# Kernel optimization log

Hardware: AMD Instinct MI355X
Metric: run time of the kernel (lower is better)

The kernel has to match this reference:

```python
import jax, jax.numpy as jnp
import numpy as np

N, K, M, DIN, DOUT = 4096, 16, 65536, 256, 256


def setup_inputs() -> dict:
    key = jax.random.key(0)
    ks = jax.random.split(key, 16)
    s = 1.0 / np.sqrt(DOUT)
    x = jax.random.normal(ks[0], (N, DIN), jnp.float32)
    h_tensor = jax.random.normal(ks[1], (M, DOUT), jnp.float32)
    c_tensor = jax.random.normal(ks[2], (M, DOUT), jnp.float32)
    # variable-length child lists: lengths in [1, K], -1 padding like get_nums()
    lengths = jax.random.randint(ks[3], (N,), 1, K + 1)
    idx = jax.random.randint(ks[4], (N, K), 0, M)
    t = jnp.arange(K)[None, :]
    indice = jnp.where(t < lengths[:, None], idx, -1).astype(jnp.int32)
    W_w = jax.random.normal(ks[5], (4 * DOUT, DIN), jnp.float32) * s
    W_b = jax.random.normal(ks[6], (4 * DOUT,), jnp.float32) * s
    h0 = jax.random.normal(ks[7], (4, DOUT), jnp.float32)
    c0 = jax.random.normal(ks[8], (4, DOUT), jnp.float32)
    Wih = jax.random.normal(ks[9], (4, 2, 4 * DOUT, DOUT), jnp.float32) * s
    Whh = jax.random.normal(ks[10], (4, 2, 4 * DOUT, DOUT), jnp.float32) * s
    bih = jax.random.normal(ks[11], (4, 2, 4 * DOUT), jnp.float32) * s
    bhh = jax.random.normal(ks[12], (4, 2, 4 * DOUT), jnp.float32) * s
    fc = jax.random.normal(ks[13], (4, DOUT, 2 * DOUT), jnp.float32) * s
    return dict(x=x, h_tensor=h_tensor, c_tensor=c_tensor, indice=indice,
                W_w=W_w, W_b=W_b, h0=h0, c0=c0, Wih=Wih, Whh=Whh,
                bih=bih, bhh=bhh, fc=fc)


def _lstm_dir(xseq, mask, h_init, c_init, W_ih, W_hh, b, reverse):
    """Masked LSTM over child axis. xseq [N,K,d], mask [N,K] bool. Mimics
    pack_padded_sequence: state frozen and output 0 at padded steps."""
    d = h_init.shape[-1]
    xs = jnp.swapaxes(xseq, 0, 1)   # [K,N,d]
    ms = jnp.swapaxes(mask, 0, 1)   # [K,N]

    def step(carry, inp):
        h, c = carry
        xt, mt = inp
        g = xt @ W_ih.T + h @ W_hh.T + b        # [N,4d], gate order i,f,g,o
        i = jax.nn.sigmoid(g[:, :d])
        f = jax.nn.sigmoid(g[:, d:2 * d])
        u = jnp.tanh(g[:, 2 * d:3 * d])
        o = jax.nn.sigmoid(g[:, 3 * d:])
        c_new = f * c + i * u
        h_new = o * jnp.tanh(c_new)
        m = mt[:, None]
        return (jnp.where(m, h_new, h), jnp.where(m, c_new, c)), jnp.where(m, h_new, 0.0)

    _, ys = jax.lax.scan(step, (h_init, c_init), (xs, ms), reverse=reverse)
    return jnp.swapaxes(ys, 0, 1)   # [N,K,d]


def _bilstm_seq(xseq, mask, h0j, c0j, Wihj, Whhj, bihj, bhhj, fcj):
    n = xseq.shape[0]
    h_init = jnp.broadcast_to(h0j, (n, h0j.shape[-1]))
    c_init = jnp.broadcast_to(c0j, (n, c0j.shape[-1]))
    yf = _lstm_dir(xseq, mask, h_init, c_init, Wihj[0], Whhj[0], bihj[0] + bhhj[0], False)
    yb = _lstm_dir(xseq, mask, h_init, c_init, Wihj[1], Whhj[1], bihj[1] + bhhj[1], True)
    y = jnp.concatenate([yf, yb], axis=-1)      # [N,K,2d]
    return jnp.einsum('nkh,dh->nkd', y, fcj)    # fc (no bias); 0 stays 0 at pads


def reference(x, h_tensor, c_tensor, indice, W_w, W_b, h0, c0, Wih, Whh, bih, bhh, fc):
    mask = indice != -1                           # [N,K]
    length = mask.sum(axis=1)                     # [N], >= 1
    safe_idx = jnp.where(mask, indice, 0)
    h = h_tensor[safe_idx]                        # [N,K,d] gather of child states
    c = c_tensor[safe_idx]
    Wx = x @ W_w.T + W_b                          # [N,4d]
    d = DOUT
    Wf, Wi, Wu, Wo = Wx[:, :d], Wx[:, d:2 * d], Wx[:, 2 * d:3 * d], Wx[:, 3 * d:]
    ys = [_bilstm_seq(h, mask, h0[j], c0[j], Wih[j], Whh[j], bih[j], bhh[j], fc[j])
          for j in range(4)]                      # U_f, U_i, U_u, U_o
    # forget branch: per-child gate, masked sum over children
    branch_f_k = jax.nn.sigmoid(Wf[:, None, :] + ys[0])
    branch_f = jnp.sum(branch_f_k * c * mask[..., None], axis=1)
    # i/u/o use last valid timestep (packed LSTM y_last)
    ar = jnp.arange(x.shape[0])
    last = length - 1
    branch_i = jax.nn.sigmoid(ys[1][ar, last] + Wi)
    branch_u = jnp.tanh(ys[2][ar, last] + Wu)
    branch_o = jax.nn.sigmoid(ys[3][ar, last] + Wo)
    new_c = branch_i * branch_u + branch_f
    new_h = branch_o * jnp.tanh(new_c)
    return new_h, new_c
```

## Files before the change

### kernel.cpp

```cpp
#include <hip/hip_runtime.h>
#include <math.h>

#define N_SEQ 4096
#define KCH   16
#define DM    256
#define G4    1024
#define LP    40
#define EP    68

typedef __attribute__((ext_vector_type(8))) short bf8;
typedef __attribute__((ext_vector_type(4))) float f4;

__device__ __forceinline__ float fast_rcp(float x) { return __builtin_amdgcn_rcpf(x); }
__device__ __forceinline__ float sigf(float x)   { return fast_rcp(1.f + __expf(-x)); }
__device__ __forceinline__ float tanh_f(float x) { return 1.f - 2.f * fast_rcp(1.f + __expf(2.f * x)); }

__device__ __forceinline__ float bf2f(unsigned short u) {
    return __uint_as_float(((unsigned)u) << 16);
}
__device__ __forceinline__ unsigned short f2bf(float f) {
    unsigned u = __float_as_uint(f);
    unsigned r = (u + 0x7fffu + ((u >> 16) & 1u)) >> 16;
    return (unsigned short)r;
}
__device__ __forceinline__ unsigned pack2(float a, float b) {
    return (unsigned)f2bf(a) | ((unsigned)f2bf(b) << 16);
}

#define GLDS(gp, lp) __builtin_amdgcn_global_load_lds( \
    (const __attribute__((address_space(1))) void*)(gp), \
    (__attribute__((address_space(3))) void*)(lp), 16, 0, 0)

#define VW(n) asm volatile("s_waitcnt vmcnt(" #n ")" ::: "memory")

template<int NSEG, int LDB>
__device__ __forceinline__ void pass_pipe(
    const unsigned short* const (&segA)[NSEG],
    const unsigned short* const (&segB)[NSEG],
    unsigned short* SM,
    f4 (&acc)[4][4], int wave, int wm, int wn, int jq, int fr)
{
    constexpr int NS = NSEG * 8;
    constexpr int L  = 4;
    constexpr int NP = (NS < L) ? NS : L;

#pragma unroll
    for (int p = 0; p < NP; ++p) {
        const unsigned short* A_ = segA[p >> 3] + (p & 7) * 32;
        const unsigned short* B_ = segB[p >> 3] + (p & 7) * 32;
        unsigned short* a = SM + (p % 5) * 8192 + wave * 1024;
        unsigned short* b = a + 4096;
        GLDS(A_, a);        GLDS(A_ + 16 * DM, a + 512);
        GLDS(B_, b);        GLDS(B_ + 16 * LDB, b + 512);
    }
#pragma unroll
    for (int t = 0; t < NS; ++t) {
        const int rem = NS - 1 - t;
        if (rem >= 3)      VW(12);
        else if (rem == 2) VW(8);
        else if (rem == 1) VW(4);
        else               VW(0);
        __builtin_amdgcn_s_barrier();

        if (t + L < NS) {
            const int tn = t + L;
            const unsigned short* A_ = segA[tn >> 3] + (tn & 7) * 32;
            const unsigned short* B_ = segB[tn >> 3] + (tn & 7) * 32;
            unsigned short* a = SM + (tn % 5) * 8192 + wave * 1024;
            unsigned short* b = a + 4096;
            GLDS(A_, a);    GLDS(A_ + 16 * DM, a + 512);
            GLDS(B_, b);    GLDS(B_ + 16 * LDB, b + 512);
        }

        const unsigned short* Ab = SM + (t % 5) * 8192;
        const unsigned short* Bb = Ab + 4096;
        bf8 af[4], bb[4];
#pragma unroll
        for (int i = 0; i < 4; ++i)
            af[i] = *(const bf8*)(Ab + (wm + i * 16 + fr) * 32 + jq);
#pragma unroll
        for (int j = 0; j < 4; ++j)
            bb[j] = *(const bf8*)(Bb + (wn + j * 16 + fr) * 32 + jq);

        __builtin_amdgcn_s_setprio(1);
#pragma unroll
        for (int i = 0; i < 4; ++i)
#pragma unroll
            for (int j = 0; j < 4; ++j)
                acc[i][j] = __builtin_amdgcn_mfma_f32_16x16x32_bf16(
                    af[i], bb[j], acc[i][j], 0, 0, 0);
        __builtin_amdgcn_s_setprio(0);
    }
}

template<int KLEN>
__device__ __forceinline__ void pass_bf(
    const unsigned short* __restrict__ aRow,
    const unsigned short* __restrict__ bRow,
    unsigned short* Asm, unsigned short* Bsm, f4 (&acc)[4][4])
{
    const int tid  = threadIdx.x;
    const int kh   = (tid & 1) * 16;
    const int srow = tid >> 1;
    const int lane = tid & 63, wave = tid >> 6;
    const int wm = (wave >> 1) * 64, wn = (wave & 1) * 64;
    const int fr = lane & 15, fk = (lane >> 4) * 8;
    unsigned short* da = Asm + srow * LP + kh;
    unsigned short* db = Bsm + srow * LP + kh;

    for (int k0 = 0; k0 < KLEN; k0 += 32) {
        __syncthreads();
        *(int4*)(da)     = *(const int4*)(aRow + k0 + kh);
        *(int4*)(da + 8) = *(const int4*)(aRow + k0 + kh + 8);
        *(int4*)(db)     = *(const int4*)(bRow + k0 + kh);
        *(int4*)(db + 8) = *(const int4*)(bRow + k0 + kh + 8);
        __syncthreads();
        bf8 af[4], bb[4];
#pragma unroll
        for (int i = 0; i < 4; ++i)
            af[i] = *(const bf8*)(Asm + (wm + i * 16 + fr) * LP + fk);
#pragma unroll
        for (int j = 0; j < 4; ++j)
            bb[j] = *(const bf8*)(Bsm + (wn + j * 16 + fr) * LP + fk);
#pragma unroll
        for (int i = 0; i < 4; ++i)
#pragma unroll
            for (int j = 0; j < 4; ++j)
                acc[i][j] = __builtin_amdgcn_mfma_f32_16x16x32_bf16(
                    af[i], bb[j], acc[i][j], 0, 0, 0);
    }
}

template<int KLEN>
__device__ __forceinline__ void pass_f32(
    const float* __restrict__ aRow,
    const unsigned short* __restrict__ bRow,
    unsigned short* Asm, unsigned short* Bsm, f4 (&acc)[4][4])
{
    const int tid  = threadIdx.x;
    const int kh   = (tid & 1) * 16;
    const int srow = tid >> 1;
    const int lane = tid & 63, wave = tid >> 6;
    const int wm = (wave >> 1) * 64, wn = (wave & 1) * 64;
    const int fr = lane & 15, fk = (lane >> 4) * 8;
    unsigned short* da = Asm + srow * LP + kh;
    unsigned short* db = Bsm + srow * LP + kh;

    for (int k0 = 0; k0 < KLEN; k0 += 32) {
        __syncthreads();
        {
            const float* s = aRow + k0 + kh;
            float4 v0 = *(const float4*)(s);
            float4 v1 = *(const float4*)(s + 4);
            float4 v2 = *(const float4*)(s + 8);
            float4 v3 = *(const float4*)(s + 12);
            *(int4*)(da)     = make_int4(pack2(v0.x, v0.y), pack2(v0.z, v0.w),
                                         pack2(v1.x, v1.y), pack2(v1.z, v1.w));
            *(int4*)(da + 8) = make_int4(pack2(v2.x, v2.y), pack2(v2.z, v2.w),
                                         pack2(v3.x, v3.y), pack2(v3.z, v3.w));
        }
        *(int4*)(db)     = *(const int4*)(bRow + k0 + kh);
        *(int4*)(db + 8) = *(const int4*)(bRow + k0 + kh + 8);
        __syncthreads();
        bf8 af[4], bb[4];
#pragma unroll
        for (int i = 0; i < 4; ++i)
            af[i] = *(const bf8*)(Asm + (wm + i * 16 + fr) * LP + fk);
#pragma unroll
        for (int j = 0; j < 4; ++j)
            bb[j] = *(const bf8*)(Bsm + (wn + j * 16 + fr) * LP + fk);
#pragma unroll
        for (int i = 0; i < 4; ++i)
#pragma unroll
            for (int j = 0; j < 4; ++j)
                acc[i][j] = __builtin_amdgcn_mfma_f32_16x16x32_bf16(
                    af[i], bb[j], acc[i][j], 0, 0, 0);
    }
}


__global__ __launch_bounds__(256) void k_lastidx(
    const int* __restrict__ indice, int* __restrict__ last_idx)
{
    const int n = blockIdx.x * 256 + threadIdx.x;
    if (n >= N_SEQ) return;
    int len = 0;
#pragma unroll
    for (int k = 0; k < KCH; ++k) len += (indice[n * KCH + k] != -1);
    last_idx[n] = indice[n * KCH + (len - 1)];
}

__global__ __launch_bounds__(1024) void k_hh0_bsum2(
    const float* __restrict__ bih, const float* __restrict__ bhh,
    const float* __restrict__ h0, const float* __restrict__ Whh,
    float* __restrict__ bsum2)
{
    const int jz = blockIdx.x, j = jz + 1;
    const int g = threadIdx.x;
    const int jd = j * 2 + 1;
    const float* wrow = Whh + ((size_t)jd * G4 + g) * DM;
    float s = bih[jd * G4 + g] + bhh[jd * G4 + g];
    for (int h = 0; h < DM; ++h) s = fmaf(h0[j * DM + h], wrow[h], s);
    const int c = (g & 255) * 4 + (g >> 8);
    bsum2[jz * G4 + c] = s;
}

__global__ __launch_bounds__(256) void k_init_states(
    const float* __restrict__ h0, const float* __restrict__ c0,
    unsigned short* __restrict__ hA, float* __restrict__ c_state)
{
    const int row = blockIdx.x;
    const int s = row >> 12;
    const int tree = (s < 4) ? s : 0;
    const int d = threadIdx.x;
    hA[(size_t)row * DM + d]      = f2bf(h0[tree * DM + d]);
    c_state[(size_t)row * DM + d] = c0[tree * DM + d];
}

__global__ __launch_bounds__(256) void k_zero4(float4* __restrict__ p)
{
    p[(size_t)blockIdx.x * 256 + threadIdx.x] = make_float4(0.f, 0.f, 0.f, 0.f);
}

__global__ __launch_bounds__(256) void k_prep_wcat(
    const float* __restrict__ Wih, const float* __restrict__ Whh,
    const float* __restrict__ bih, const float* __restrict__ bhh,
    unsigned short* __restrict__ wcat, float* __restrict__ bsumr)
{
    const int c = blockIdx.x, s = blockIdx.y;
    const int wsel = (s < 4) ? s * 2 : 1;
    const int d = c >> 2, g = c & 3;
    const size_t srcrow = ((size_t)wsel * G4 + g * DM + d) * DM;
    unsigned short* dst = wcat + ((size_t)s * G4 + c) * 512;
    const int t = threadIdx.x;
    dst[t]       = f2bf(Wih[srcrow + t]);
    dst[256 + t] = f2bf(Whh[srcrow + t]);
    if (t == 0)
        bsumr[s * G4 + c] = bih[wsel * G4 + g * DM + d] + bhh[wsel * G4 + g * DM + d];
}

__global__ __launch_bounds__(256) void k_prep_wcat2(
    const float* __restrict__ Wih, unsigned short* __restrict__ wcat2)
{
    const int c = blockIdx.x, jz = blockIdx.y, j = jz + 1;
    const int d = c >> 2, g = c & 3;
    const size_t srcrow = ((size_t)(j * 2 + 1) * G4 + g * DM + d) * DM;
    wcat2[((size_t)jz * G4 + c) * 256 + threadIdx.x] = f2bf(Wih[srcrow + threadIdx.x]);
}

__global__ __launch_bounds__(256) void k_prep_fcb(
    const float* __restrict__ fc, unsigned short* __restrict__ fcb)
{
    const int dout = blockIdx.x, z = blockIdx.y, t = threadIdx.x;
    fcb[((size_t)z * DM + dout) * DM + t] = f2bf(fc[(size_t)dout * 512 + z * DM + t]);
}

__global__ __launch_bounds__(256) void k_prep_fcb2(
    const float* __restrict__ fc, unsigned short* __restrict__ fcb2)
{
    const int dout = blockIdx.x, jz = blockIdx.y, j = jz + 1, t = threadIdx.x;
    const float* src = fc + ((size_t)j * DM + dout) * 512;
    unsigned short* dst = fcb2 + ((size_t)jz * DM + dout) * 512;
    dst[t]       = f2bf(src[t]);
    dst[t + 256] = f2bf(src[t + 256]);
}

__global__ __launch_bounds__(256) void k_prep_wwb(
    const float* __restrict__ W_w, unsigned short* __restrict__ wwb)
{
    const size_t i = (size_t)blockIdx.x * 256 + threadIdx.x;
    wwb[i] = f2bf(W_w[i]);
}

__device__ __forceinline__ void gather_slice(
    const float* __restrict__ h_tensor, const int* __restrict__ indice,
    unsigned short* __restrict__ xbuf, int zz, int kk, int blk)
{
    const int row = blk * 64 + (threadIdx.x >> 2);
    const int cb  = (threadIdx.x & 3) * 64;
    int idx = indice[row * KCH + kk]; if (idx < 0) idx = 0;
    const float* src = h_tensor + (size_t)idx * DM + cb;
    unsigned short* dst = xbuf + ((size_t)zz * N_SEQ + row) * DM + cb;
#pragma unroll
    for (int c = 0; c < 64; c += 4) {
        float4 v = *(const float4*)(src + c);
        *(uint2*)(dst + c) = make_uint2(pack2(v.x, v.y), pack2(v.z, v.w));
    }
}

__global__ __launch_bounds__(256) void k_gather_x0(
    const float* __restrict__ h_tensor, const int* __restrict__ indice,
    unsigned short* __restrict__ xbuf)
{
    const int slice = blockIdx.x >> 6, blk = blockIdx.x & 63;
    gather_slice(h_tensor, indice, xbuf, slice, slice ? (KCH - 1) : 0, blk);
}

__global__ __launch_bounds__(256) void k_scan_merged(
    const unsigned short* __restrict__ xb_cur, unsigned short* __restrict__ xb_nxt,
    const unsigned short* __restrict__ yb_prev, unsigned short* __restrict__ yb_cur,
    const int* __restrict__ indice, const float* __restrict__ h_tensor,
    const unsigned short* __restrict__ h_in, unsigned short* __restrict__ h_out,
    float* __restrict__ c_state,
    const unsigned short* __restrict__ wcat, const float* __restrict__ bsumr,
    const unsigned short* __restrict__ fcb, unsigned short* __restrict__ ys0,
    int r)
{
    __shared__ __align__(16) unsigned short SMEM[40960];

    const int tid  = threadIdx.x;
    const int lane = tid & 63, wave = tid >> 6;
    const int wm = (wave >> 1) * 64, wn = (wave & 1) * 64;
    const int fr = lane & 15;
    const int jq = ((lane >> 4) ^ ((fr >> 1) & 3)) * 8;
    const int lr = wave * 32 + (lane >> 2);
    const int jl = ((lane & 3) ^ ((lane >> 3) & 3)) * 8;

    const int bz = blockIdx.z;

    if (bz == 5) {
        const int id5 = blockIdx.x + 8 * blockIdx.y;
        if (id5 >= 128) {
            const int rr = r + 1;
            if (rr >= KCH) return;
            const int g = id5 - 128;
            const int zz = g >> 6;
            gather_slice(h_tensor, indice, xb_nxt, zz,
                         zz ? (KCH - 1 - rr) : rr, g & 63);
            return;
        }
        if (r == 0) return;
        const int rp = r - 1;
        const int z = id5 >> 6;
        const int kslice = z ? (KCH - 1 - rp) : rp;
        const int row0 = (id5 & 31) * 128;
        const int c0 = ((id5 >> 5) & 1) * 128;

        const unsigned short* ay0 = yb_prev + ((size_t)z * N_SEQ + row0 + lr) * DM + jl;
        const unsigned short* bf0 = fcb + ((size_t)z * DM + c0 + lr) * DM + jl;

        f4 acc[4][4];
#pragma unroll
        for (int i = 0; i < 4; ++i)
#pragma unroll
            for (int j = 0; j < 4; ++j) acc[i][j] = (f4)(0.f);
        {
            const unsigned short* const segA[1] = { ay0 };
            const unsigned short* const segB[1] = { bf0 };
            pass_pipe<1, 256>(segA, segB, SMEM, acc, wave, wm, wn, jq, fr);
        }

#pragma unroll
        for (int i = 0; i < 4; ++i)
#pragma unroll
            for (int j = 0; j < 4; ++j) {
                const int col = c0 + wn + j * 16 + fr;
#pragma unroll
                for (int reg = 0; reg < 4; ++reg) {
                    const int rowg = row0 + wm + i * 16 + (lane >> 4) * 4 + reg;
                    const size_t ix = ((size_t)rowg * KCH + kslice) * DM + col;
                    ys0[ix] = f2bf(bf2f(ys0[ix]) + acc[i][j][reg]);
                }
            }
        return;
    }

    const int s = bz;
    const int k = (s < 4) ? r : (KCH - 1 - r);
    const int z = (s < 4) ? 0 : 1;
    const int bn = blockIdx.y & 7;
    const int bm = (blockIdx.y >> 3) * 8 + blockIdx.x;
    const int row0 = bm * 128, c0 = bn * 128;

    const unsigned short* xz = xb_cur + (size_t)z * N_SEQ * DM;
    const unsigned short* hs_in = h_in + (size_t)s * N_SEQ * DM;
    const unsigned short* ax0 = xz + (size_t)(row0 + lr) * DM + jl;
    const unsigned short* ah0 = hs_in + (size_t)(row0 + lr) * DM + jl;
    const unsigned short* bw0 = wcat + ((size_t)s * G4 + c0 + lr) * 512 + jl;

    f4 acc[4][4];
#pragma unroll
    for (int i = 0; i < 4; ++i)
#pragma unroll
        for (int j = 0; j < 4; ++j) acc[i][j] = (f4)(0.f);

    {
        const unsigned short* const segA[2] = { ax0, ah0 };
        const unsigned short* const segB[2] = { bw0, bw0 + 256 };
        pass_pipe<2, 512>(segA, segB, SMEM, acc, wave, wm, wn, jq, fr);
    }

    float* sc = (float*)SMEM + wave * (16 * EP);
    __syncthreads();
    const int kprev = (s < 4) ? (k - 1) : (k + 1);
    const int dq = lane & 15;
    const int rq = lane >> 4;
#pragma unroll
    for (int i = 0; i < 4; ++i) {
#pragma unroll
        for (int j = 0; j < 4; ++j) {
            const int colL = j * 16 + fr;
            const int rbase = (lane >> 4) * 4;
#pragma unroll
            for (int reg = 0; reg < 4; ++reg)
                sc[(rbase + reg) * EP + colL] = acc[i][j][reg];
        }
        asm volatile("s_waitcnt lgkmcnt(0)" ::: "memory");
        __builtin_amdgcn_sched_barrier(0);
#pragma unroll
        for (int q = 0; q < 4; ++q) {
            const int rloc = rq + q * 4;
            const int rowg = row0 + wm + i * 16 + rloc;
            const bool m = (indice[rowg * KCH + k] != -1);
            const bool mpv = (r == 0) ? true : (indice[rowg * KCH + kprev] != -1);
            const f4 gv = *(const f4*)(sc + rloc * EP + dq * 4);
            const f4 bb = *(const f4*)(bsumr + s * G4 + c0 + wn + dq * 4);
            const int d = ((c0 + wn) >> 2) + dq;
            const size_t cix = ((size_t)s * N_SEQ + rowg) * DM + d;
            unsigned short hv = 0;
            if (m) {
                const float ii = sigf(gv.x + bb.x);
                const float ff = sigf(gv.y + bb.y);
                const float uu = tanh_f(gv.z + bb.z);
                const float oo = sigf(gv.w + bb.w);
                const float c_old = c_state[cix];
                const float cn = ff * c_old + ii * uu;
                c_state[cix] = cn;
                hv = f2bf(oo * tanh_f(cn));
                h_out[cix] = hv;
            } else if (mpv) {
                h_out[cix] = hs_in[(size_t)rowg * DM + d];
            }
            if (s == 0)
                yb_cur[(size_t)rowg * DM + d] = m ? hv : (unsigned short)0;
            else if (s == 4)
                yb_cur[(size_t)(N_SEQ + rowg) * DM + d] = m ? hv : (unsigned short)0;
        }
        asm volatile("s_waitcnt lgkmcnt(0)" ::: "memory");
        __builtin_amdgcn_sched_barrier(0);
    }
}

__global__ __launch_bounds__(256) void k_acc_tail(
    const unsigned short* __restrict__ ybuf, const unsigned short* __restrict__ fcb,
    unsigned short* __restrict__ ys0)
{
    __shared__ __align__(16) unsigned short SMEM[40960];
    const int tid = threadIdx.x;
    const int lane = tid & 63, wave = tid >> 6;
    const int wm = (wave >> 1) * 64, wn = (wave & 1) * 64;
    const int fr = lane & 15;
    const int jq = ((lane >> 4) ^ ((fr >> 1) & 3)) * 8;
    const int lr = wave * 32 + (lane >> 2);
    const int jl = ((lane & 3) ^ ((lane >> 3) & 3)) * 8;

    const int z = blockIdx.z;
    const int kslice = z ? 0 : (KCH - 1);
    const int row0 = blockIdx.y * 128, c0 = blockIdx.x * 128;

    const unsigned short* ay0 = ybuf + ((size_t)z * N_SEQ + row0 + lr) * DM + jl;
    const unsigned short* bf0 = fcb + ((size_t)z * DM + c0 + lr) * DM + jl;

    f4 acc[4][4];
#pragma unroll
    for (int i = 0; i < 4; ++i)
#pragma unroll
        for (int j = 0; j < 4; ++j) acc[i][j] = (f4)(0.f);
    {
        const unsigned short* const segA[1] = { ay0 };
        const unsigned short* const segB[1] = { bf0 };
        pass_pipe<1, 256>(segA, segB, SMEM, acc, wave, wm, wn, jq, fr);
    }

#pragma unroll
    for (int i = 0; i < 4; ++i)
#pragma unroll
        for (int j = 0; j < 4; ++j) {
            const int col = c0 + wn + j * 16 + fr;
#pragma unroll
            for (int reg = 0; reg < 4; ++reg) {
                const int rowg = row0 + wm + i * 16 + (lane >> 4) * 4 + reg;
                const size_t ix = ((size_t)rowg * KCH + kslice) * DM + col;
                ys0[ix] = f2bf(bf2f(ys0[ix]) + acc[i][j][reg]);
            }
        }
}


__global__ __launch_bounds__(256) void k_bwd_mfma(
    const float* __restrict__ h_tensor, const int* __restrict__ last_idx,
    const unsigned short* __restrict__ wcat2, const float* __restrict__ bsum2,
    const float* __restrict__ c0, unsigned short* __restrict__ yb_last)
{
    __shared__ __align__(16) unsigned short SMEM[2 * 128 * LP];
    const int jz = blockIdx.z, j = jz + 1;
    const int row0 = blockIdx.y * 128, c0t = blockIdx.x * 128;
    const int tid = threadIdx.x;
    const int srow = tid >> 1;

    const float* aF = h_tensor + (size_t)last_idx[row0 + srow] * DM;
    const unsigned short* bR = wcat2 + ((size_t)jz * G4 + c0t + srow) * 256;

    f4 acc[4][4];
#pragma unroll
    for (int i = 0; i < 4; ++i)
#pragma unroll
        for (int jj = 0; jj < 4; ++jj) acc[i][jj] = (f4)(0.f);

    pass_f32<256>(aF, bR, SMEM, SMEM + 128 * LP, acc);

    const int lane = tid & 63, wave = tid >> 6;
    const int wm = (wave >> 1) * 64, wn = (wave & 1) * 64;
    float* sc = (float*)SMEM + wave * (16 * EP);

    __syncthreads();
#pragma unroll
    for (int i = 0; i < 4; ++i) {
#pragma unroll
        for (int jj = 0; jj < 4; ++jj) {
            const int colL = jj * 16 + (lane & 15);
            const int rbase = (lane >> 4) * 4;
#pragma unroll
            for (int reg = 0; reg < 4; ++reg)
                sc[(rbase + reg) * EP + colL] = acc[i][jj][reg];
        }
        __syncthreads();
        const int rowg = row0 + wm + i * 16 + (lane & 15);
#pragma unroll
        for (int q = 0; q < 4; ++q) {
            const int dL = (lane >> 4) + q * 4;
            const f4 gv = *(const f4*)(sc + (lane & 15) * EP + dL * 4);
            const f4 bb = *(const f4*)(bsum2 + jz * G4 + c0t + wn + dL * 4);
            const int d = ((c0t + wn) >> 2) + dL;
            const float ii = sigf(gv.x + bb.x);
            const float ff = sigf(gv.y + bb.y);
            const float uu = tanh_f(gv.z + bb.z);
            const float oo = sigf(gv.w + bb.w);
            const float cn = ff * c0[j * DM + d] + ii * uu;
            yb_last[((size_t)jz * N_SEQ + rowg) * DM + d] = f2bf(oo * tanh_f(cn));
        }
        __syncthreads();
    }
}

__global__ __launch_bounds__(256) void k_wx_mfma(
    const float* __restrict__ x, const unsigned short* __restrict__ wwb,
    const float* __restrict__ W_b, unsigned short* __restrict__ Wx)
{
    __shared__ __align__(16) unsigned short SMEM[2 * 128 * LP];
    const int row0 = blockIdx.y * 128, c0 = blockIdx.x * 128;
    const int tid = threadIdx.x;
    const int srow = tid >> 1;

    const float* aF = x + (size_t)(row0 + srow) * DM;
    const unsigned short* bR = wwb + (size_t)(c0 + srow) * DM;

    f4 acc[4][4];
#pragma unroll
    for (int i = 0; i < 4; ++i)
#pragma unroll
        for (int j = 0; j < 4; ++j) acc[i][j] = (f4)(0.f);

    pass_f32<256>(aF, bR, SMEM, SMEM + 128 * LP, acc);

    const int lane = tid & 63, wave = tid >> 6;
    const int wm = (wave >> 1) * 64, wn = (wave & 1) * 64;
#pragma unroll
    for (int i = 0; i < 4; ++i)
#pragma unroll
        for (int j = 0; j < 4; ++j) {
            const int col = c0 + wn + j * 16 + (lane & 15);
            const float bv = W_b[col];
#pragma unroll
            for (int reg = 0; reg < 4; ++reg) {
                const int rowg = row0 + wm + i * 16 + (lane >> 4) * 4 + reg;
                Wx[(size_t)rowg * G4 + col] = f2bf(acc[i][j][reg] + bv);
            }
        }
}

__global__ __launch_bounds__(256) void k_fc_last_mfma(
    const unsigned short* __restrict__ h_final, const unsigned short* __restrict__ yb_last,
    const unsigned short* __restrict__ fcb2, unsigned short* __restrict__ ys_last)
{
    __shared__ __align__(16) unsigned short SMEM[2 * 128 * LP];
    const int jz = blockIdx.z;
    const int row0 = blockIdx.y * 128, c0 = blockIdx.x * 128;
    const int tid = threadIdx.x;
    const int srow = tid >> 1;

    const unsigned short* aH1 = h_final + ((size_t)(1 + jz) * N_SEQ + row0 + srow) * DM;
    const unsigned short* aH2 = yb_last + ((size_t)jz * N_SEQ + row0 + srow) * DM;
    const unsigned short* bR  = fcb2 + ((size_t)jz * DM + c0 + srow) * 512;

    f4 acc[4][4];
#pragma unroll
    for (int i = 0; i < 4; ++i)
#pragma unroll
        for (int j = 0; j < 4; ++j) acc[i][j] = (f4)(0.f);

    pass_bf<256>(aH1, bR, SMEM, SMEM + 128 * LP, acc);
    pass_bf<256>(aH2, bR + 256, SMEM, SMEM + 128 * LP, acc);

    const int lane = tid & 63, wave = tid >> 6;
    const int wm = (wave >> 1) * 64, wn = (wave & 1) * 64;
#pragma unroll
    for (int i = 0; i < 4; ++i)
#pragma unroll
        for (int j = 0; j < 4; ++j) {
            const int col = c0 + wn + j * 16 + (lane & 15);
#pragma unroll
            for (int reg = 0; reg < 4; ++reg) {
                const int rowg = row0 + wm + i * 16 + (lane >> 4) * 4 + reg;
                ys_last[((size_t)jz * N_SEQ + rowg) * DM + col] = f2bf(acc[i][j][reg]);
            }
        }
}

__global__ __launch_bounds__(256) void k_final(
    const unsigned short* __restrict__ Wx, const unsigned short* __restrict__ ys0,
    const unsigned short* __restrict__ ys_last, const float* __restrict__ c_tensor,
    const int* __restrict__ indice, float* __restrict__ out)
{
    const int n = blockIdx.x, d = threadIdx.x;
    const float Wf = bf2f(Wx[(size_t)n * G4 + d]);
    const float Wi = bf2f(Wx[(size_t)n * G4 + DM + d]);
    const float Wu = bf2f(Wx[(size_t)n * G4 + 2 * DM + d]);
    const float Wo = bf2f(Wx[(size_t)n * G4 + 3 * DM + d]);
    float bf = 0.f;
#pragma unroll
    for (int k = 0; k < KCH; ++k) {
        const int id = indice[n * KCH + k];
        if (id >= 0)
            bf += sigf(Wf + bf2f(ys0[((size_t)n * KCH + k) * DM + d])) *
                  c_tensor[(size_t)id * DM + d];
    }
    const float bi = sigf(bf2f(ys_last[((size_t)0 * N_SEQ + n) * DM + d]) + Wi);
    const float bu = tanh_f(bf2f(ys_last[((size_t)1 * N_SEQ + n) * DM + d]) + Wu);
    const float bo = sigf(bf2f(ys_last[((size_t)2 * N_SEQ + n) * DM + d]) + Wo);
    const float nc = bi * bu + bf;
    const float nh = bo * tanh_f(nc);
    out[(size_t)n * DM + d] = nh;
    out[(size_t)N_SEQ * DM + (size_t)n * DM + d] = nc;
}

extern "C" void kernel_launch(void* const* d_in, const int* in_sizes, int n_in,
                              void* d_out, int out_size, void* d_ws, size_t ws_size,
                              hipStream_t stream)
{
    const float* x        = (const float*)d_in[0];
    const float* h_tensor = (const float*)d_in[1];
    const float* c_tensor = (const float*)d_in[2];
    const int*   indice   = (const int*)d_in[3];
    const float* W_w      = (const float*)d_in[4];
    const float* W_b      = (const float*)d_in[5];
    const float* h0       = (const float*)d_in[6];
    const float* c0       = (const float*)d_in[7];
    const float* Wih      = (const float*)d_in[8];
    const float* Whh      = (const float*)d_in[9];
    const float* bih      = (const float*)d_in[10];
    const float* bhh      = (const float*)d_in[11];
    const float* fc       = (const float*)d_in[12];
    float* out = (float*)d_out;

    char* base = (char*)d_ws;
    float*          c_state  = (float*)(base + 0);
    int*            last_idx = (int*)  (base + 20971520);
    float*          bsumr    = (float*)(base + 20987904);
    unsigned short* hA       = (unsigned short*)(base + 21008384);
    unsigned short* hB       = (unsigned short*)(base + 31494144);
    unsigned short* ys0      = (unsigned short*)(base + 41979904);
    unsigned short* ybufA    = (unsigned short*)(base + 75534336);
    unsigned short* ybufB    = (unsigned short*)(base + 79728640);
    unsigned short* xbufA    = (unsigned short*)(base + 83922944);
    unsigned short* fcb      = (unsigned short*)(base + 88117248);
    unsigned short* postbuf  = (unsigned short*)(base + 88379392);
    unsigned short* wcat     = (unsigned short*)(base + 92573696);
    const size_t need = 97816576;
    if (ws_size < need) return;

    unsigned short* xbufB   = postbuf;
    unsigned short* wcat2   = postbuf;
    unsigned short* fcb2    = postbuf + 786432;
    unsigned short* wwb     = postbuf + 1179648;
    float*          bsum2   = (float*)(postbuf + 1441792);
    unsigned short* yb_last = ybufA;
    unsigned short* ys_last = hB;
    unsigned short* WxBuf   = hA;

    k_lastidx<<<16, 256, 0, stream>>>(indice, last_idx);
    k_init_states<<<5 * N_SEQ, 256, 0, stream>>>(h0, c0, hA, c_state);
    k_zero4<<<8192, 256, 0, stream>>>((float4*)ys0);
    k_prep_wcat<<<dim3(G4, 5), 256, 0, stream>>>(Wih, Whh, bih, bhh, wcat, bsumr);
    k_prep_fcb<<<dim3(DM, 2), 256, 0, stream>>>(fc, fcb);
    k_gather_x0<<<128, 256, 0, stream>>>(h_tensor, indice, xbufA);

    for (int r = 0; r < KCH; ++r) {
        const unsigned short* xb_cur = (r & 1) ? xbufB : xbufA;
        unsigned short* xb_nxt       = (r & 1) ? xbufA : xbufB;
        const unsigned short* yb_prev = (r & 1) ? ybufA : ybufB;
        unsigned short* yb_cur        = (r & 1) ? ybufB : ybufA;
        const unsigned short* h_in = (r & 1) ? hB : hA;
        unsigned short* h_out      = (r & 1) ? hA : hB;
        k_scan_merged<<<dim3(8, 32, 6), 256, 0, stream>>>(
            xb_cur, xb_nxt, yb_prev, yb_cur, indice, h_tensor,
            h_in, h_out, c_state, wcat, bsumr, fcb, ys0, r);
    }

    k_acc_tail<<<dim3(2, 32, 2), 256, 0, stream>>>(ybufB, fcb, ys0);

    k_prep_wcat2<<<dim3(G4, 3), 256, 0, stream>>>(Wih, wcat2);
    k_hh0_bsum2<<<3, 1024, 0, stream>>>(bih, bhh, h0, Whh, bsum2);
    k_prep_fcb2<<<dim3(DM, 3), 256, 0, stream>>>(fc, fcb2);
    k_prep_wwb<<<1024, 256, 0, stream>>>(W_w, wwb);

    k_bwd_mfma<<<dim3(8, 32, 3), 256, 0, stream>>>(
        h_tensor, last_idx, wcat2, bsum2, c0, yb_last);
    k_fc_last_mfma<<<dim3(2, 32, 3), 256, 0, stream>>>(hA, yb_last, fcb2, ys_last);
    k_wx_mfma<<<dim3(8, 32), 256, 0, stream>>>(x, wwb, W_b, WxBuf);

    k_final<<<N_SEQ, 256, 0, stream>>>(WxBuf, ys0, ys_last, c_tensor, indice, out);
}
```

Before: 1.213 ms.

## Switch recurrent LSTM scan GEMMs to FP8 MFMA with scaled operands

Stores the gathered child inputs, hidden states and concatenated LSTM weights as scaled FP8 (e4m3) instead of bf16, and runs the main recurrent gate GEMM with the fp8 16x16x32 MFMA. Gate results are rescaled by a constant. Final hidden states are also written as bf16 into a separate buffer for the later fc kernel. The fc-accumulate pass moves to a simpler double-buffered pipeline. This halves operand bandwidth and LDS traffic in the 16-step scan, at the cost of lower numerical precision in the recurrence, which may exceed tolerance.

After: 1.298 ms. 7.0% more time.

```diff
diff --git a/kernel.cpp b/kernel.cpp
--- a/kernel.cpp
+++ b/kernel.cpp
@@ -7,6 +7,7 @@
 #define G4    1024
 #define LP    40
 #define EP    68
+#define GSC   0.0078125f
 
 typedef __attribute__((ext_vector_type(8))) short bf8;
 typedef __attribute__((ext_vector_type(4))) float f4;
@@ -26,12 +27,131 @@
 __device__ __forceinline__ unsigned pack2(float a, float b) {
     return (unsigned)f2bf(a) | ((unsigned)f2bf(b) << 16);
 }
+__device__ __forceinline__ unsigned char f2fp8(float x) {
+    return (unsigned char)(__builtin_amdgcn_cvt_pk_fp8_f32(x, 0.f, 0, false) & 0xff);
+}
+__device__ __forceinline__ unsigned pack4fp8(float a, float b, float c, float d) {
+    unsigned p = __builtin_amdgcn_cvt_pk_fp8_f32(a, b, 0, false);
+    return __builtin_amdgcn_cvt_pk_fp8_f32(c, d, p, true);
+}
+__device__ __forceinline__ float fp8dec(unsigned char u) {
+    const int e = (u >> 3) & 15, m = u & 7;
+    float v = (e == 0) ? (float)m * 0.001953125f
+                       : (float)(8 + m) * __uint_as_float((unsigned)(e + 117) << 23);
+    return (u & 0x80) ? -v : v;
+}
 
 #define GLDS(gp, lp) __builtin_amdgcn_global_load_lds( \
     (const __attribute__((address_space(1))) void*)(gp), \
     (__attribute__((address_space(3))) void*)(lp), 16, 0, 0)
 
 #define VW(n) asm volatile("s_waitcnt vmcnt(" #n ")" ::: "memory")
+
+template<int NSEG>
+__device__ __forceinline__ void pass_pipe8(
+    const unsigned char* const (&segA)[NSEG],
+    const unsigned char* const (&segB)[NSEG],
+    unsigned char* SM8,
+    f4 (&acc)[4][4], int wave, int wm, int wn, int lane)
+{
+    constexpr int NS = NSEG * 8;
+    constexpr int L  = 4;
+    constexpr int NP = (NS < L) ? NS : L;
+    const int fr = lane & 15, kh = (lane >> 4) * 8;
+
+#pragma unroll
+    for (int p = 0; p < NP; ++p) {
+        const unsigned char* A_ = segA[p >> 3] + (p & 7) * 32;
+        const unsigned char* B_ = segB[p >> 3] + (p & 7) * 32;
+        unsigned char* a = SM8 + (p % 5) * 8192 + wave * 1024;
+        unsigned char* b = a + 4096;
+        GLDS(A_, a);  GLDS(B_, b);
+    }
+#pragma unroll
+    for (int t = 0; t < NS; ++t) {
+        const int rem = NS - 1 - t;
+        if (rem >= 3)      VW(6);
+        else if (rem == 2) VW(4);
+        else if (rem == 1) VW(2);
+        else               VW(0);
+        __builtin_amdgcn_s_barrier();
+
+        if (t + L < NS) {
+            const int tn = t + L;
+            const unsigned char* A_ = segA[tn >> 3] + (tn & 7) * 32;
+            const unsigned char* B_ = segB[tn >> 3] + (tn & 7) * 32;
+            unsigned char* a = SM8 + (tn % 5) * 8192 + wave * 1024;
+            unsigned char* b = a + 4096;
+            GLDS(A_, a);  GLDS(B_, b);
+        }
+
+        const unsigned char* Ab = SM8 + (t % 5) * 8192;
+        const unsigned char* Bb = Ab + 4096;
+        long af[4], bb[4];
+#pragma unroll
+        for (int i = 0; i < 4; ++i)
+            af[i] = *(const long*)(Ab + (wm + i * 16 + fr) * 32 + kh);
+#pragma unroll
+        for (int j = 0; j < 4; ++j)
+            bb[j] = *(const long*)(Bb + (wn + j * 16 + fr) * 32 + kh);
+
+        __builtin_amdgcn_s_setprio(1);
+#pragma unroll
+        for (int i = 0; i < 4; ++i)
+#pragma unroll
+            for (int j = 0; j < 4; ++j)
+                acc[i][j] = __builtin_amdgcn_mfma_f32_16x16x32_fp8_fp8(
+                    af[i], bb[j], acc[i][j], 0, 0, 0);
+        __builtin_amdgcn_s_setprio(0);
+    }
+}
+
+template<int NSEG, int LDB>
+__device__ __forceinline__ void pass_pipe2(
+    const unsigned short* const (&segA)[NSEG],
+    const unsigned short* const (&segB)[NSEG],
+    unsigned short* SM,
+    f4 (&acc)[4][4], int wave, int wm, int wn, int jq, int fr)
+{
+    constexpr int NS = NSEG * 8;
+    {
+        const unsigned short* A_ = segA[0];
+        const unsigned short* B_ = segB[0];
+        unsigned short* a = SM + wave * 1024;
+        unsigned short* b = a + 4096;
+        GLDS(A_, a);        GLDS(A_ + 16 * DM, a + 512);
+        GLDS(B_, b);        GLDS(B_ + 16 * LDB, b + 512);
+    }
+#pragma unroll
+    for (int t = 0; t < NS; ++t) {
+        VW(0);
+        __builtin_amdgcn_s_barrier();
+        if (t + 1 < NS) {
+            const int tn = t + 1;
+            const unsigned short* A_ = segA[tn >> 3] + (tn & 7) * 32;
+            const unsigned short* B_ = segB[tn >> 3] + (tn & 7) * 32;
+            unsigned short* a = SM + (tn & 1) * 8192 + wave * 1024;
+            unsigned short* b = a + 4096;
+            GLDS(A_, a);    GLDS(A_ + 16 * DM, a + 512);
+            GLDS(B_, b);    GLDS(B_ + 16 * LDB, b + 512);
+        }
+        const unsigned short* Ab = SM + (t & 1) * 8192;
+        const unsigned short* Bb = Ab + 4096;
+        bf8 af[4], bb[4];
+#pragma unroll
+        for (int i = 0; i < 4; ++i)
+            af[i] = *(const bf8*)(Ab + (wm + i * 16 + fr) * 32 + jq);
+#pragma unroll
+        for (int j = 0; j < 4; ++j)
+            bb[j] = *(const bf8*)(Bb + (wn + j * 16 + fr) * 32 + jq);
+#pragma unroll
+        for (int i = 0; i < 4; ++i)
+#pragma unroll
+            for (int j = 0; j < 4; ++j)
+                acc[i][j] = __builtin_amdgcn_mfma_f32_16x16x32_bf16(
+                    af[i], bb[j], acc[i][j], 0, 0, 0);
+    }
+}
 
 template<int NSEG, int LDB>
 __device__ __forceinline__ void pass_pipe(
@@ -43,7 +163,6 @@
     constexpr int NS = NSEG * 8;
     constexpr int L  = 4;
     constexpr int NP = (NS < L) ? NS : L;
-
 #pragma unroll
     for (int p = 0; p < NP; ++p) {
         const unsigned short* A_ = segA[p >> 3] + (p & 7) * 32;
@@ -61,7 +180,6 @@
         else if (rem == 1) VW(4);
         else               VW(0);
         __builtin_amdgcn_s_barrier();
-
         if (t + L < NS) {
             const int tn = t + L;
             const unsigned short* A_ = segA[tn >> 3] + (tn & 7) * 32;
@@ -71,7 +189,6 @@
             GLDS(A_, a);    GLDS(A_ + 16 * DM, a + 512);
             GLDS(B_, b);    GLDS(B_ + 16 * LDB, b + 512);
         }
-
         const unsigned short* Ab = SM + (t % 5) * 8192;
         const unsigned short* Bb = Ab + 4096;
         bf8 af[4], bb[4];
@@ -81,7 +198,6 @@
 #pragma unroll
         for (int j = 0; j < 4; ++j)
             bb[j] = *(const bf8*)(Bb + (wn + j * 16 + fr) * 32 + jq);
-
         __builtin_amdgcn_s_setprio(1);
 #pragma unroll
         for (int i = 0; i < 4; ++i)
@@ -207,13 +323,13 @@
 
 __global__ __launch_bounds__(256) void k_init_states(
     const float* __restrict__ h0, const float* __restrict__ c0,
-    unsigned short* __restrict__ hA, float* __restrict__ c_state)
+    unsigned char* __restrict__ hA8, float* __restrict__ c_state)
 {
     const int row = blockIdx.x;
     const int s = row >> 12;
     const int tree = (s < 4) ? s : 0;
     const int d = threadIdx.x;
-    hA[(size_t)row * DM + d]      = f2bf(h0[tree * DM + d]);
+    hA8[(size_t)row * DM + d]     = f2fp8(h0[tree * DM + d] * 8.f);
     c_state[(size_t)row * DM + d] = c0[tree * DM + d];
 }
 
@@ -225,16 +341,16 @@
 __global__ __launch_bounds__(256) void k_prep_wcat(
     const float* __restrict__ Wih, const float* __restrict__ Whh,
     const float* __restrict__ bih, const float* __restrict__ bhh,
-    unsigned short* __restrict__ wcat, float* __restrict__ bsumr)
+    unsigned char* __restrict__ wcat8, float* __restrict__ bsumr)
 {
     const int c = blockIdx.x, s = blockIdx.y;
     const int wsel = (s < 4) ? s * 2 : 1;
     const int d = c >> 2, g = c & 3;
     const size_t srcrow = ((size_t)wsel * G4 + g * DM + d) * DM;
-    unsigned short* dst = wcat + ((size_t)s * G4 + c) * 512;
+    unsigned char* dst = wcat8 + ((size_t)s * G4 + c) * 512;
     const int t = threadIdx.x;
-    dst[t]       = f2bf(Wih[srcrow + t]);
-    dst[256 + t] = f2bf(Whh[srcrow + t]);
+    dst[t]       = f2fp8(Wih[srcrow + t] * 16.f);
+    dst[256 + t] = f2fp8(Whh[srcrow + t] * 16.f);
     if (t == 0)
         bsumr[s * G4 + c] = bih[wsel * G4 + g * DM + d] + bhh[wsel * G4 + g * DM + d];
 }
@@ -272,49 +388,51 @@
     wwb[i] = f2bf(W_w[i]);
 }
 
-__device__ __forceinline__ void gather_slice(
+__device__ __forceinline__ void gather_slice8(
     const float* __restrict__ h_tensor, const int* __restrict__ indice,
-    unsigned short* __restrict__ xbuf, int zz, int kk, int blk)
+    unsigned char* __restrict__ xbuf, int zz, int kk, int blk)
 {
     const int row = blk * 64 + (threadIdx.x >> 2);
     const int cb  = (threadIdx.x & 3) * 64;
     int idx = indice[row * KCH + kk]; if (idx < 0) idx = 0;
     const float* src = h_tensor + (size_t)idx * DM + cb;
-    unsigned short* dst = xbuf + ((size_t)zz * N_SEQ + row) * DM + cb;
-#pragma unroll
-    for (int c = 0; c < 64; c += 4) {
-        float4 v = *(const float4*)(src + c);
-        *(uint2*)(dst + c) = make_uint2(pack2(v.x, v.y), pack2(v.z, v.w));
+    unsigned char* dst = xbuf + ((size_t)zz * N_SEQ + row) * DM + cb;
+#pragma unroll
+    for (int c = 0; c < 64; c += 16) {
+        unsigned q[4];
+#pragma unroll
+        for (int u = 0; u < 4; ++u) {
+            float4 v = *(const float4*)(src + c + u * 4);
+            q[u] = pack4fp8(v.x * 8.f, v.y * 8.f, v.z * 8.f, v.w * 8.f);
+        }
+        *(uint4*)(dst + c) = make_uint4(q[0], q[1], q[2], q[3]);
     }
 }
 
 __global__ __launch_bounds__(256) void k_gather_x0(
     const float* __restrict__ h_tensor, const int* __restrict__ indice,
-    unsigned short* __restrict__ xbuf)
+    unsigned char* __restrict__ xbuf)
 {
     const int slice = blockIdx.x >> 6, blk = blockIdx.x & 63;
-    gather_slice(h_tensor, indice, xbuf, slice, slice ? (KCH - 1) : 0, blk);
+    gather_slice8(h_tensor, indice, xbuf, slice, slice ? (KCH - 1) : 0, blk);
 }
 
 __global__ __launch_bounds__(256) void k_scan_merged(
-    const unsigned short* __restrict__ xb_cur, unsigned short* __restrict__ xb_nxt,
+    const unsigned char* __restrict__ xb_cur, unsigned char* __restrict__ xb_nxt,
     const unsigned short* __restrict__ yb_prev, unsigned short* __restrict__ yb_cur,
     const int* __restrict__ indice, const float* __restrict__ h_tensor,
-    const unsigned short* __restrict__ h_in, unsigned short* __restrict__ h_out,
+    const unsigned char* __restrict__ h_in, unsigned char* __restrict__ h_out,
     float* __restrict__ c_state,
-    const unsigned short* __restrict__ wcat, const float* __restrict__ bsumr,
+    const unsigned char* __restrict__ wcat8, const float* __restrict__ bsumr,
     const unsigned short* __restrict__ fcb, unsigned short* __restrict__ ys0,
-    int r)
-{
-    __shared__ __align__(16) unsigned short SMEM[40960];
+    unsigned short* __restrict__ hfin, int r)
+{
+    __shared__ __align__(16) unsigned char SMEM8[40960];
 
     const int tid  = threadIdx.x;
     const int lane = tid & 63, wave = tid >> 6;
     const int wm = (wave >> 1) * 64, wn = (wave & 1) * 64;
     const int fr = lane & 15;
-    const int jq = ((lane >> 4) ^ ((fr >> 1) & 3)) * 8;
-    const int lr = wave * 32 + (lane >> 2);
-    const int jl = ((lane & 3) ^ ((lane >> 3) & 3)) * 8;
 
     const int bz = blockIdx.z;
 
@@ -325,11 +443,15 @@
             if (rr >= KCH) return;
             const int g = id5 - 128;
             const int zz = g >> 6;
-            gather_slice(h_tensor, indice, xb_nxt, zz,
-                         zz ? (KCH - 1 - rr) : rr, g & 63);
+            gather_slice8(h_tensor, indice, xb_nxt, zz,
+                          zz ? (KCH - 1 - rr) : rr, g & 63);
             return;
         }
         if (r == 0) return;
+        const int jq = ((lane >> 4) ^ ((fr >> 1) & 3)) * 8;
+        const int lr = wave * 32 + (lane >> 2);
+        const int jl = ((lane & 3) ^ ((lane >> 3) & 3)) * 8;
+        unsigned short* SMS = (unsigned short*)SMEM8;
         const int rp = r - 1;
         const int z = id5 >> 6;
         const int kslice = z ? (KCH - 1 - rp) : rp;
@@ -347,9 +469,8 @@
         {
             const unsigned short* const segA[1] = { ay0 };
             const unsigned short* const segB[1] = { bf0 };
-            pass_pipe<1, 256>(segA, segB, SMEM, acc, wave, wm, wn, jq, fr);
-        }
-
+            pass_pipe2<1, 256>(segA, segB, SMS, acc, wave, wm, wn, jq, fr);
+        }
 #pragma unroll
         for (int i = 0; i < 4; ++i)
 #pragma unroll
@@ -372,11 +493,13 @@
     const int bm = (blockIdx.y >> 3) * 8 + blockIdx.x;
     const int row0 = bm * 128, c0 = bn * 128;
 
-    const unsigned short* xz = xb_cur + (size_t)z * N_SEQ * DM;
-    const unsigned short* hs_in = h_in + (size_t)s * N_SEQ * DM;
-    const unsigned short* ax0 = xz + (size_t)(row0 + lr) * DM + jl;
-    const unsigned short* ah0 = hs_in + (size_t)(row0 + lr) * DM + jl;
-    const unsigned short* bw0 = wcat + ((size_t)s * G4 + c0 + lr) * 512 + jl;
+    const int lr8 = wave * 32 + (lane >> 1);
+    const int ch8 = (lane & 1) * 16;
+    const unsigned char* xz = xb_cur + (size_t)z * N_SEQ * DM;
+    const unsigned char* hs_in = h_in + (size_t)s * N_SEQ * DM;
+    const unsigned char* ax0 = xz + (size_t)(row0 + lr8) * DM + ch8;
+    const unsigned char* ah0 = hs_in + (size_t)(row0 + lr8) * DM + ch8;
+    const unsigned char* bw0 = wcat8 + ((size_t)s * G4 + c0 + lr8) * 512 + ch8;
 
     f4 acc[4][4];
 #pragma unroll
@@ -385,16 +508,17 @@
         for (int j = 0; j < 4; ++j) acc[i][j] = (f4)(0.f);
 
     {
-        const unsigned short* const segA[2] = { ax0, ah0 };
-        const unsigned short* const segB[2] = { bw0, bw0 + 256 };
-        pass_pipe<2, 512>(segA, segB, SMEM, acc, wave, wm, wn, jq, fr);
-    }
-
-    float* sc = (float*)SMEM + wave * (16 * EP);
+        const unsigned char* const segA[2] = { ax0, ah0 };
+        const unsigned char* const segB[2] = { bw0, bw0 + 256 };
+        pass_pipe8<2>(segA, segB, SMEM8, acc, wave, wm, wn, lane);
+    }
+
+    float* sc = (float*)SMEM8 + wave * (16 * EP);
     __syncthreads();
     const int kprev = (s < 4) ? (k - 1) : (k + 1);
     const int dq = lane & 15;
     const int rq = lane >> 4;
+    const bool fin = (r == KCH - 1) && (s >= 1) && (s < 4);
 #pragma unroll
     for (int i = 0; i < 4; ++i) {
 #pragma unroll
@@ -417,24 +541,31 @@
             const f4 bb = *(const f4*)(bsumr + s * G4 + c0 + wn + dq * 4);
             const int d = ((c0 + wn) >> 2) + dq;
             const size_t cix = ((size_t)s * N_SEQ + rowg) * DM + d;
-            unsigned short hv = 0;
+            unsigned short yv = 0;
             if (m) {
-                const float ii = sigf(gv.x + bb.x);
-                const float ff = sigf(gv.y + bb.y);
-                const float uu = tanh_f(gv.z + bb.z);
-                const float oo = sigf(gv.w + bb.w);
+                const float ii = sigf(gv.x * GSC + bb.x);
+                const float ff = sigf(gv.y * GSC + bb.y);
+                const float uu = tanh_f(gv.z * GSC + bb.z);
+                const float oo = sigf(gv.w * GSC + bb.w);
                 const float c_old = c_state[cix];
                 const float cn = ff * c_old + ii * uu;
                 c_state[cix] = cn;
-                hv = f2bf(oo * tanh_f(cn));
-                h_out[cix] = hv;
-            } else if (mpv) {
-                h_out[cix] = hs_in[(size_t)rowg * DM + d];
+                const float hn = oo * tanh_f(cn);
+                h_out[cix] = f2fp8(hn * 8.f);
+                yv = f2bf(hn);
+                if (fin)
+                    hfin[((size_t)(s - 1) * N_SEQ + rowg) * DM + d] = yv;
+            } else if (mpv || fin) {
+                const unsigned char hb = hs_in[(size_t)rowg * DM + d];
+                if (mpv) h_out[cix] = hb;
+                if (fin)
+                    hfin[((size_t)(s - 1) * N_SEQ + rowg) * DM + d] =
+                        f2bf(fp8dec(hb) * 0.125f);
             }
             if (s == 0)
-                yb_cur[(size_t)rowg * DM + d] = m ? hv : (unsigned short)0;
+                yb_cur[(size_t)rowg * DM + d] = m ? yv : (unsigned short)0;
             else if (s == 4)
-                yb_cur[(size_t)(N_SEQ + rowg) * DM + d] = m ? hv : (unsigned short)0;
+                yb_cur[(size_t)(N_SEQ + rowg) * DM + d] = m ? yv : (unsigned short)0;
         }
         asm volatile("s_waitcnt lgkmcnt(0)" ::: "memory");
         __builtin_amdgcn_sched_barrier(0);
@@ -471,7 +602,6 @@
         const unsigned short* const segB[1] = { bf0 };
         pass_pipe<1, 256>(segA, segB, SMEM, acc, wave, wm, wn, jq, fr);
     }
-
 #pragma unroll
     for (int i = 0; i < 4; ++i)
 #pragma unroll
@@ -580,7 +710,7 @@
 }
 
 __global__ __launch_bounds__(256) void k_fc_last_mfma(
-    const unsigned short* __restrict__ h_final, const unsigned short* __restrict__ yb_last,
+    const unsigned short* __restrict__ hfin, const unsigned short* __restrict__ yb_last,
     const unsigned short* __restrict__ fcb2, unsigned short* __restrict__ ys_last)
 {
     __shared__ __align__(16) unsigned short SMEM[2 * 128 * LP];
@@ -589,7 +719,7 @@
     const int tid = threadIdx.x;
     const int srow = tid >> 1;
 
-    const unsigned short* aH1 = h_final + ((size_t)(1 + jz) * N_SEQ + row0 + srow) * DM;
+    const unsigned short* aH1 = hfin + ((size_t)jz * N_SEQ + row0 + srow) * DM;
     const unsigned short* aH2 = yb_last + ((size_t)jz * N_SEQ + row0 + srow) * DM;
     const unsigned short* bR  = fcb2 + ((size_t)jz * DM + c0 + srow) * 512;
 
@@ -667,44 +797,45 @@
     float*          c_state  = (float*)(base + 0);
     int*            last_idx = (int*)  (base + 20971520);
     float*          bsumr    = (float*)(base + 20987904);
-    unsigned short* hA       = (unsigned short*)(base + 21008384);
-    unsigned short* hB       = (unsigned short*)(base + 31494144);
+    unsigned char*  hA8      = (unsigned char*)(base + 21008384);
+    unsigned char*  hB8      = (unsigned char*)(base + 26251264);
+    unsigned short* hfin     = (unsigned short*)(base + 31494144);
     unsigned short* ys0      = (unsigned short*)(base + 41979904);
     unsigned short* ybufA    = (unsigned short*)(base + 75534336);
     unsigned short* ybufB    = (unsigned short*)(base + 79728640);
-    unsigned short* xbufA    = (unsigned short*)(base + 83922944);
+    unsigned char*  xbufA8   = (unsigned char*)(base + 83922944);
+    unsigned char*  xbufB8   = (unsigned char*)(base + 86020096);
     unsigned short* fcb      = (unsigned short*)(base + 88117248);
     unsigned short* postbuf  = (unsigned short*)(base + 88379392);
-    unsigned short* wcat     = (unsigned short*)(base + 92573696);
+    unsigned char*  wcat8    = (unsigned char*)(base + 92573696);
     const size_t need = 97816576;
     if (ws_size < need) return;
 
-    unsigned short* xbufB   = postbuf;
     unsigned short* wcat2   = postbuf;
     unsigned short* fcb2    = postbuf + 786432;
     unsigned short* wwb     = postbuf + 1179648;
     float*          bsum2   = (float*)(postbuf + 1441792);
     unsigned short* yb_last = ybufA;
-    unsigned short* ys_last = hB;
-    unsigned short* WxBuf   = hA;
+    unsigned short* ys_last = (unsigned short*)(base + 21008384);
+    unsigned short* WxBuf   = (unsigned short*)(base + 27299840);
 
     k_lastidx<<<16, 256, 0, stream>>>(indice, last_idx);
-    k_init_states<<<5 * N_SEQ, 256, 0, stream>>>(h0, c0, hA, c_state);
+    k_init_states<<<5 * N_SEQ, 256, 0, stream>>>(h0, c0, hA8, c_state);
     k_zero4<<<8192, 256, 0, stream>>>((float4*)ys0);
-    k_prep_wcat<<<dim3(G4, 5), 256, 0, stream>>>(Wih, Whh, bih, bhh, wcat, bsumr);
+    k_prep_wcat<<<dim3(G4, 5), 256, 0, stream>>>(Wih, Whh, bih, bhh, wcat8, bsumr);
     k_prep_fcb<<<dim3(DM, 2), 256, 0, stream>>>(fc, fcb);
-    k_gather_x0<<<128, 256, 0, stream>>>(h_tensor, indice, xbufA);
+    k_gather_x0<<<128, 256, 0, stream>>>(h_tensor, indice, xbufA8);
 
     for (int r = 0; r < KCH; ++r) {
-        const unsigned short* xb_cur = (r & 1) ? xbufB : xbufA;
-        unsigned short* xb_nxt       = (r & 1) ? xbufA : xbufB;
+        const unsigned char* xb_cur = (r & 1) ? xbufB8 : xbufA8;
+        unsigned char* xb_nxt       = (r & 1) ? xbufA8 : xbufB8;
         const unsigned short* yb_prev = (r & 1) ? ybufA : ybufB;
         unsigned short* yb_cur        = (r & 1) ? ybufB : ybufA;
-        const unsigned short* h_in = (r & 1) ? hB : hA;
-        unsigned short* h_out      = (r & 1) ? hA : hB;
+        const unsigned char* h_in = (r & 1) ? hB8 : hA8;
+        unsigned char* h_out      = (r & 1) ? hA8 : hB8;
         k_scan_merged<<<dim3(8, 32, 6), 256, 0, stream>>>(
             xb_cur, xb_nxt, yb_prev, yb_cur, indice, h_tensor,
-            h_in, h_out, c_state, wcat, bsumr, fcb, ys0, r);
+            h_in, h_out, c_state, wcat8, bsumr, fcb, ys0, hfin, r);
     }
 
     k_acc_tail<<<dim3(2, 32, 2), 256, 0, stream>>>(ybufB, fcb, ys0);
@@ -716,7 +847,7 @@
 
     k_bwd_mfma<<<dim3(8, 32, 3), 256, 0, stream>>>(
         h_tensor, last_idx, wcat2, bsum2, c0, yb_last);
-    k_fc_last_mfma<<<dim3(2, 32, 3), 256, 0, stream>>>(hA, yb_last, fcb2, ys_last);
+    k_fc_last_mfma<<<dim3(2, 32, 3), 256, 0, stream>>>(hfin, yb_last, fcb2, ys_last);
     k_wx_mfma<<<dim3(8, 32), 256, 0, stream>>>(x, wwb, W_b, WxBuf);
 
     k_final<<<N_SEQ, 256, 0, stream>>>(WxBuf, ys0, ys_last, c_tensor, indice, out);
```
